# Kernel tuning notes

Hardware: AMD Instinct MI355X
Metric: run time of the kernel (lower is better)

The kernel has to match this reference:

```python
import jax, jax.numpy as jnp
import numpy as np

V0, V1, C = 64, 128, 128
V = V0 * V1  # product-graph node count = kron eigenvalue count


def setup_inputs() -> dict:
    key = jax.random.key(0)
    ks = jax.random.split(key, 8)
    x = jax.random.normal(ks[0], (V, C), dtype=jnp.float32)
    edge_index = jax.random.randint(ks[1], (2, 100), 0, V)  # unused on spectral path
    L = jnp.zeros((2, 2), dtype=jnp.float32)                # unused on spectral path
    mass = jax.random.uniform(ks[2], (V,), dtype=jnp.float32) + 0.5  # positive lumped mass
    evals0 = jax.random.uniform(ks[3], (V0,), dtype=jnp.float32) * 2.0  # factor-graph eigenvalues >= 0
    evals1 = jax.random.uniform(ks[4], (V1,), dtype=jnp.float32) * 2.0
    evecs = jax.random.normal(ks[5], (V, V), dtype=jnp.float32) / np.float32(np.sqrt(V))
    diffusion_time = jax.random.uniform(ks[6], (2, C), dtype=jnp.float32)  # nn.Parameter [P, C_inout]
    return {
        "x": x, "edge_index": edge_index, "L": L, "mass": mass,
        "evals0": evals0, "evals1": evals1, "evecs": evecs,
        "diffusion_time": diffusion_time,
    }


def reference(x, edge_index, L, mass, evals0, evals1, evecs, diffusion_time):
    # to_basis: project mass-weighted signal onto the spectral basis. [V,C]
    x_spec = evecs.T @ (x * mass[:, None])
    # Per-channel Kronecker diffusion coefficients:
    # kron(exp(-t0[c]*evals0), exp(-t1[c]*evals1)) for each channel c.
    e0 = jnp.exp(-evals0[:, None] * diffusion_time[0][None, :])  # [V0, C]
    e1 = jnp.exp(-evals1[:, None] * diffusion_time[1][None, :])  # [V1, C]
    diffusion_coefs = (e0[:, None, :] * e1[None, :, :]).reshape(V0 * V1, C)  # [V, C]
    # from_basis: back to node domain.
    x_diffuse = evecs @ (diffusion_coefs * x_spec)
    return x_diffuse
```

## Files before the change

### kernel.cpp

```cpp
#include <hip/hip_runtime.h>
#include <hip/hip_bf16.h>
#include <stdint.h>

#define V 8192
#define C 128
#define KS 8
#define KCH (V / KS)
#define BK 64
#define NI (KCH / BK)

typedef __attribute__((ext_vector_type(8))) short short8;
typedef __attribute__((ext_vector_type(4))) float floatx4;

static __device__ __forceinline__ unsigned short f2bf(float f) {
    unsigned u = __float_as_uint(f);
    u += 0x7FFF + ((u >> 16) & 1);
    return (unsigned short)(u >> 16);
}

__global__ __launch_bounds__(256) void prep_xmt(const float* __restrict__ x,
                                                const float* __restrict__ mass,
                                                unsigned short* __restrict__ XMT) {
    __shared__ float tile[64][65];
    const int k0 = blockIdx.x * 64;
    const int c0 = blockIdx.y * 64;
    const int t = threadIdx.x;
#pragma unroll
    for (int p = 0; p < 16; ++p) {
        int idx = p * 256 + t;
        int kk = idx >> 6, cc = idx & 63;
        tile[kk][cc] = x[(size_t)(k0 + kk) * C + (c0 + cc)] * mass[k0 + kk];
    }
    __syncthreads();
#pragma unroll
    for (int p = 0; p < 16; ++p) {
        int idx = p * 256 + t;
        int cc = idx >> 6, kk = idx & 63;
        XMT[(size_t)(c0 + cc) * V + (k0 + kk)] = f2bf(tile[kk][cc]);
    }
}

#define MFMA_BODY                                                                   \
    {                                                                               \
        _Pragma("unroll")                                                           \
        for (int kk = 0; kk < BK; kk += 32) {                                       \
            short8 af[4], bf[4];                                                    \
            _Pragma("unroll")                                                       \
            for (int mi = 0; mi < 4; ++mi) {                                        \
                int m = wm + mi * 16 + l15;                                         \
                int cpos = ((kk >> 3) + q) ^ (m & 7);                               \
                af[mi] = *(const short8*)&ldsA[m * BK + 8 * cpos];                  \
            }                                                                       \
            _Pragma("unroll")                                                       \
            for (int ni = 0; ni < 4; ++ni) {                                        \
                int n = wn + ni * 16 + l15;                                         \
                int cpos = ((kk >> 3) + q) ^ (n & 7);                               \
                bf[ni] = *(const short8*)&ldsB[n * BK + 8 * cpos];                  \
            }                                                                       \
            _Pragma("unroll")                                                       \
            for (int mi = 0; mi < 4; ++mi)                                          \
                _Pragma("unroll")                                                   \
                for (int ni = 0; ni < 4; ++ni)                                      \
                    acc[mi][ni] = __builtin_amdgcn_mfma_f32_16x16x32_bf16(          \
                        af[mi], bf[ni], acc[mi][ni], 0, 0, 0);                      \
        }                                                                           \
    }

__global__ __launch_bounds__(256, 2) void gemm1_fused(const unsigned short* __restrict__ XMT,
                                                      const float* __restrict__ E,
                                                      float* __restrict__ P1) {
    __shared__ __align__(16) unsigned short ldsA[128 * BK];
    __shared__ __align__(16) unsigned short ldsB[128 * BK];
    const int bx = blockIdx.x;
    const int ks = bx & (KS - 1);
    const int n0 = (bx >> 3) * 128;
    const int kb = ks * KCH;
    const int t = threadIdx.x;
    const int w = t >> 6, lane = t & 63, q = lane >> 4, l15 = lane & 15;
    const int wm = (w & 1) * 64, wn = (w >> 1) * 64;
    const int acp = t & 7;
    const int ar8 = t >> 3;
    const int jg = (t & 7) | ((t >> 6) << 3);
    const int vq = (t >> 3) & 7;

    floatx4 acc[4][4] = {};
    float4 e0[8], e1[8];

#pragma unroll
    for (int rr = 0; rr < 8; ++rr)
        e0[rr] = *(const float4*)&E[(size_t)(kb + vq * 8 + rr) * V + n0 + jg * 4];

    for (int it = 0; it < NI; it += 2) {
        const int k0 = kb + it * BK;
        const int k1 = k0 + BK;
        const int kp = (k1 + BK < kb + KCH) ? (k1 + BK) : (kb + KCH - BK);
        __syncthreads();
        uint4 br[4];
#pragma unroll
        for (int u = 0; u < 4; ++u)
            br[u] = *(const uint4*)&XMT[(size_t)(ar8 + 32 * u) * V + k0 + acp * 8];
#pragma unroll
        for (int rr = 0; rr < 8; ++rr)
            e1[rr] = *(const float4*)&E[(size_t)(k1 + vq * 8 + rr) * V + n0 + jg * 4];
#pragma unroll
        for (int u = 0; u < 4; ++u) {
            int r = ar8 + 32 * u;
            *(uint4*)&ldsA[r * BK + ((acp ^ (r & 7))) * 8] = br[u];
        }
        {
            const float* lf = (const float*)e0;
#pragma unroll
            for (int jj = 0; jj < 4; ++jj) {
                int j = jg * 4 + jj;
                short8 b;
#pragma unroll
                for (int rr = 0; rr < 8; ++rr) b[rr] = (short)f2bf(lf[rr * 4 + jj]);
                *(short8*)&ldsB[j * BK + (vq ^ (j & 7)) * 8] = b;
            }
        }
        __syncthreads();
        MFMA_BODY;
        __syncthreads();
#pragma unroll
        for (int u = 0; u < 4; ++u)
            br[u] = *(const uint4*)&XMT[(size_t)(ar8 + 32 * u) * V + k1 + acp * 8];
#pragma unroll
        for (int rr = 0; rr < 8; ++rr)
            e0[rr] = *(const float4*)&E[(size_t)(kp + vq * 8 + rr) * V + n0 + jg * 4];
#pragma unroll
        for (int u = 0; u < 4; ++u) {
            int r = ar8 + 32 * u;
            *(uint4*)&ldsA[r * BK + ((acp ^ (r & 7))) * 8] = br[u];
        }
        {
            const float* lf = (const float*)e1;
#pragma unroll
            for (int jj = 0; jj < 4; ++jj) {
                int j = jg * 4 + jj;
                short8 b;
#pragma unroll
                for (int rr = 0; rr < 8; ++rr) b[rr] = (short)f2bf(lf[rr * 4 + jj]);
                *(short8*)&ldsB[j * BK + (vq ^ (j & 7)) * 8] = b;
            }
        }
        __syncthreads();
        MFMA_BODY;
    }
    float* Pks = P1 + (size_t)ks * C * V;
#pragma unroll
    for (int mi = 0; mi < 4; ++mi) {
        int mrow = wm + mi * 16 + q * 4;
#pragma unroll
        for (int ni = 0; ni < 4; ++ni) {
            int n = n0 + wn + ni * 16 + l15;
#pragma unroll
            for (int r = 0; r < 4; ++r)
                Pks[(size_t)(mrow + r) * V + n] = acc[mi][ni][r];
        }
    }
}

__global__ __launch_bounds__(256, 2) void gemm2_fused(const float* __restrict__ E,
                                                      const unsigned short* __restrict__ YT,
                                                      float* __restrict__ P2) {
    __shared__ __align__(16) unsigned short ldsA[128 * BK];
    __shared__ __align__(16) unsigned short ldsB[128 * BK];
    const int bx = blockIdx.x;
    const int ks = bx & (KS - 1);
    const int m0 = (bx >> 3) * 128;
    const int kb = ks * KCH;
    const int t = threadIdx.x;
    const int w = t >> 6, lane = t & 63, q = lane >> 4, l15 = lane & 15;
    const int wm = (w & 1) * 64, wn = (w >> 1) * 64;
    const int ach = t & 15;
    const int ar  = t >> 4;
    const int bcp = t & 7;
    const int br8 = t >> 3;

    floatx4 acc[4][4] = {};
    float4 e0[8], e1[8];

#pragma unroll
    for (int u = 0; u < 8; ++u)
        e0[u] = *(const float4*)&E[(size_t)(m0 + ar + 16 * u) * V + kb + ach * 4];

    for (int it = 0; it < NI; it += 2) {
        const int k0 = kb + it * BK;
        const int k1 = k0 + BK;
        const int kp = (k1 + BK < kb + KCH) ? (k1 + BK) : (kb + KCH - BK);
        __syncthreads();
        uint4 br[4];
#pragma unroll
        for (int u = 0; u < 4; ++u)
            br[u] = *(const uint4*)&YT[(size_t)(br8 + 32 * u) * V + k0 + bcp * 8];
#pragma unroll
        for (int u = 0; u < 8; ++u)
            e1[u] = *(const float4*)&E[(size_t)(m0 + ar + 16 * u) * V + k1 + ach * 4];
#pragma unroll
        for (int u = 0; u < 4; ++u) {
            int r = br8 + 32 * u;
            *(uint4*)&ldsB[r * BK + ((bcp ^ (r & 7))) * 8] = br[u];
        }
        {
            const float* lf = (const float*)e0;
#pragma unroll
            for (int u = 0; u < 8; ++u) {
                int row = ar + 16 * u;
                ushort4 av;
                av.x = f2bf(lf[u * 4 + 0]); av.y = f2bf(lf[u * 4 + 1]);
                av.z = f2bf(lf[u * 4 + 2]); av.w = f2bf(lf[u * 4 + 3]);
                *(ushort4*)&ldsA[row * BK + ((ach >> 1) ^ (row & 7)) * 8 + (ach & 1) * 4] = av;
            }
        }
        __syncthreads();
        MFMA_BODY;
        __syncthreads();
#pragma unroll
        for (int u = 0; u < 4; ++u)
            br[u] = *(const uint4*)&YT[(size_t)(br8 + 32 * u) * V + k1 + bcp * 8];
#pragma unroll
        for (int u = 0; u < 8; ++u)
            e0[u] = *(const float4*)&E[(size_t)(m0 + ar + 16 * u) * V + kp + ach * 4];
#pragma unroll
        for (int u = 0; u < 4; ++u) {
            int r = br8 + 32 * u;
            *(uint4*)&ldsB[r * BK + ((bcp ^ (r & 7))) * 8] = br[u];
        }
        {
            const float* lf = (const float*)e1;
#pragma unroll
            for (int u = 0; u < 8; ++u) {
                int row = ar + 16 * u;
                ushort4 av;
                av.x = f2bf(lf[u * 4 + 0]); av.y = f2bf(lf[u * 4 + 1]);
                av.z = f2bf(lf[u * 4 + 2]); av.w = f2bf(lf[u * 4 + 3]);
                *(ushort4*)&ldsA[row * BK + ((ach >> 1) ^ (row & 7)) * 8 + (ach & 1) * 4] = av;
            }
        }
        __syncthreads();
        MFMA_BODY;
    }
    float* Pks = P2 + (size_t)ks * V * C;
#pragma unroll
    for (int mi = 0; mi < 4; ++mi) {
        int mrow = m0 + wm + mi * 16 + q * 4;
#pragma unroll
        for (int ni = 0; ni < 4; ++ni) {
            int n = wn + ni * 16 + l15;
#pragma unroll
            for (int r = 0; r < 4; ++r)
                Pks[(size_t)(mrow + r) * C + n] = acc[mi][ni][r];
        }
    }
}

__global__ __launch_bounds__(256) void red1(const float* __restrict__ P1,
                                            const float* __restrict__ ev0,
                                            const float* __restrict__ ev1,
                                            const float* __restrict__ dt,
                                            unsigned short* __restrict__ YT) {
    int id = blockIdx.x * 256 + threadIdx.x;
    int c = id >> 10;
    int j0 = (id & 1023) * 8;
    float s[8] = {};
#pragma unroll
    for (int ks = 0; ks < KS; ++ks) {
        const float* row = &P1[((size_t)ks * C + c) * V + j0];
        float4 a = *(const float4*)row;
        float4 b = *(const float4*)(row + 4);
        s[0] += a.x; s[1] += a.y; s[2] += a.z; s[3] += a.w;
        s[4] += b.x; s[5] += b.y; s[6] += b.z; s[7] += b.w;
    }
    float t0 = dt[c], t1 = dt[C + c];
    float a0 = ev0[j0 >> 7] * t0;
    short8 yv;
#pragma unroll
    for (int jj = 0; jj < 8; ++jj) {
        float coef = __expf(-(a0 + ev1[(j0 + jj) & 127] * t1));
        yv[jj] = (short)f2bf(s[jj] * coef);
    }
    *(short8*)&YT[(size_t)c * V + j0] = yv;
}

__global__ __launch_bounds__(256) void red2(const float* __restrict__ P2,
                                            float* __restrict__ out) {
    int id = blockIdx.x * 256 + threadIdx.x;
    size_t off = (size_t)id * 4;
    float4 s = {0.f, 0.f, 0.f, 0.f};
#pragma unroll
    for (int ks = 0; ks < KS; ++ks) {
        float4 v = *(const float4*)&P2[(size_t)ks * V * C + off];
        s.x += v.x; s.y += v.y; s.z += v.z; s.w += v.w;
    }
    *(float4*)&out[off] = s;
}

extern "C" void kernel_launch(void* const* d_in, const int* in_sizes, int n_in,
                              void* d_out, int out_size, void* d_ws, size_t ws_size,
                              hipStream_t stream) {
    const float* x    = (const float*)d_in[0];
    const float* mass = (const float*)d_in[3];
    const float* ev0  = (const float*)d_in[4];
    const float* ev1  = (const float*)d_in[5];
    const float* E    = (const float*)d_in[6];
    const float* dt   = (const float*)d_in[7];
    float* out = (float*)d_out;

    unsigned short* XMT = (unsigned short*)d_ws;
    unsigned short* YT  = XMT + (size_t)V * C;
    float* P = (float*)(YT + (size_t)V * C);

    prep_xmt<<<dim3(V / 64, C / 64), 256, 0, stream>>>(x, mass, XMT);
    gemm1_fused<<<(V / 128) * KS, 256, 0, stream>>>(XMT, E, P);
    red1<<<(C * V / 8) / 256, 256, 0, stream>>>(P, ev0, ev1, dt, YT);
    gemm2_fused<<<(V / 128) * KS, 256, 0, stream>>>(E, YT, P);
    red2<<<(V * C / 4) / 256, 256, 0, stream>>>(P, out);
}
```

Baseline: 444.3 us.

## Double-buffer LDS and use direct global-to-LDS loads in both GEMMs

Both split-K GEMM kernels now keep two LDS buffers and prefetch the next K tile while MFMAs run on the current one. The bf16 operand tile is loaded with global_load_lds straight into LDS, with the XOR swizzle folded into the source address. The fp32 E tile is still staged in registers and converted after compute. The loop is rewritten with one barrier per iteration, explicit waitcnt, sched_barrier and setprio around the MFMA body, which removes the extra syncs and register staging. In exchange, LDS use per block doubles to 64 KB, which may limit occupancy.

After: 447.8 us. Within noise of the previous version (+0.8%).

```diff
diff --git a/kernel.cpp b/kernel.cpp
--- a/kernel.cpp
+++ b/kernel.cpp
@@ -1,5 +1,4 @@
 #include <hip/hip_runtime.h>
-#include <hip/hip_bf16.h>
 #include <stdint.h>
 
 #define V 8192
@@ -17,6 +16,13 @@
     u += 0x7FFF + ((u >> 16) & 1);
     return (unsigned short)(u >> 16);
 }
+
+static __device__ __forceinline__ void gload16(const void* g, void* l) {
+    __builtin_amdgcn_global_load_lds(
+        (const __attribute__((address_space(1))) void*)g,
+        (__attribute__((address_space(3))) void*)l, 16, 0, 0);
+}
+#define SWAIT(s) asm volatile("s_waitcnt " s ::: "memory")
 
 __global__ __launch_bounds__(256) void prep_xmt(const float* __restrict__ x,
                                                 const float* __restrict__ mass,
@@ -40,37 +46,37 @@
     }
 }
 
-#define MFMA_BODY                                                                   \
+#define MFMA_BODY(pA, pB)                                                           \
     {                                                                               \
         _Pragma("unroll")                                                           \
         for (int kk = 0; kk < BK; kk += 32) {                                       \
-            short8 af[4], bf[4];                                                    \
+            short8 af[4], bfv[4];                                                   \
             _Pragma("unroll")                                                       \
             for (int mi = 0; mi < 4; ++mi) {                                        \
-                int m = wm + mi * 16 + l15;                                         \
-                int cpos = ((kk >> 3) + q) ^ (m & 7);                               \
-                af[mi] = *(const short8*)&ldsA[m * BK + 8 * cpos];                  \
+                const int m = wm + mi * 16 + l15;                                   \
+                const int cpos = ((kk >> 3) + q) ^ (m & 7);                         \
+                af[mi] = *(const short8*)&pA[m * BK + 8 * cpos];                    \
             }                                                                       \
             _Pragma("unroll")                                                       \
             for (int ni = 0; ni < 4; ++ni) {                                        \
-                int n = wn + ni * 16 + l15;                                         \
-                int cpos = ((kk >> 3) + q) ^ (n & 7);                               \
-                bf[ni] = *(const short8*)&ldsB[n * BK + 8 * cpos];                  \
+                const int n = wn + ni * 16 + l15;                                   \
+                const int cpos = ((kk >> 3) + q) ^ (n & 7);                         \
+                bfv[ni] = *(const short8*)&pB[n * BK + 8 * cpos];                   \
             }                                                                       \
             _Pragma("unroll")                                                       \
             for (int mi = 0; mi < 4; ++mi)                                          \
                 _Pragma("unroll")                                                   \
                 for (int ni = 0; ni < 4; ++ni)                                      \
                     acc[mi][ni] = __builtin_amdgcn_mfma_f32_16x16x32_bf16(          \
-                        af[mi], bf[ni], acc[mi][ni], 0, 0, 0);                      \
+                        af[mi], bfv[ni], acc[mi][ni], 0, 0, 0);                     \
         }                                                                           \
     }
 
 __global__ __launch_bounds__(256, 2) void gemm1_fused(const unsigned short* __restrict__ XMT,
                                                       const float* __restrict__ E,
                                                       float* __restrict__ P1) {
-    __shared__ __align__(16) unsigned short ldsA[128 * BK];
-    __shared__ __align__(16) unsigned short ldsB[128 * BK];
+    __shared__ __align__(16) unsigned short ldsA[2][128 * BK];
+    __shared__ __align__(16) unsigned short ldsB[2][128 * BK];
     const int bx = blockIdx.x;
     const int ks = bx & (KS - 1);
     const int n0 = (bx >> 3) * 128;
@@ -78,74 +84,76 @@
     const int t = threadIdx.x;
     const int w = t >> 6, lane = t & 63, q = lane >> 4, l15 = lane & 15;
     const int wm = (w & 1) * 64, wn = (w >> 1) * 64;
-    const int acp = t & 7;
-    const int ar8 = t >> 3;
-    const int jg = (t & 7) | ((t >> 6) << 3);
-    const int vq = (t >> 3) & 7;
+    const int lr = lane >> 3;
+    const int lch = (lane & 7) ^ lr;
+    const int jg = (lane & 7) | (w << 3);
+    const int vq = lane >> 3;
 
     floatx4 acc[4][4] = {};
-    float4 e0[8], e1[8];
-
-#pragma unroll
-    for (int rr = 0; rr < 8; ++rr)
-        e0[rr] = *(const float4*)&E[(size_t)(kb + vq * 8 + rr) * V + n0 + jg * 4];
-
-    for (int it = 0; it < NI; it += 2) {
-        const int k0 = kb + it * BK;
-        const int k1 = k0 + BK;
-        const int kp = (k1 + BK < kb + KCH) ? (k1 + BK) : (kb + KCH - BK);
-        __syncthreads();
-        uint4 br[4];
-#pragma unroll
-        for (int u = 0; u < 4; ++u)
-            br[u] = *(const uint4*)&XMT[(size_t)(ar8 + 32 * u) * V + k0 + acp * 8];
+    float4 ereg[8];
+
+    {
+        const int k0 = kb;
+#pragma unroll
+        for (int i = 0; i < 4; ++i)
+            gload16(&XMT[(size_t)(i * 32 + w * 8 + lr) * V + k0 + 8 * lch],
+                    &ldsA[0][i * 2048 + w * 512]);
 #pragma unroll
         for (int rr = 0; rr < 8; ++rr)
-            e1[rr] = *(const float4*)&E[(size_t)(k1 + vq * 8 + rr) * V + n0 + jg * 4];
-#pragma unroll
-        for (int u = 0; u < 4; ++u) {
-            int r = ar8 + 32 * u;
-            *(uint4*)&ldsA[r * BK + ((acp ^ (r & 7))) * 8] = br[u];
-        }
+            ereg[rr] = *(const float4*)&E[(size_t)(k0 + vq * 8 + rr) * V + n0 + jg * 4];
+        const float* lf = (const float*)ereg;
+#pragma unroll
+        for (int jj = 0; jj < 4; ++jj) {
+            const int j = jg * 4 + jj;
+            short8 b;
+#pragma unroll
+            for (int rr = 0; rr < 8; ++rr) b[rr] = (short)f2bf(lf[rr * 4 + jj]);
+            *(short8*)&ldsB[0][j * BK + (vq ^ (j & 7)) * 8] = b;
+        }
+        SWAIT("vmcnt(0) lgkmcnt(0)");
+        __builtin_amdgcn_s_barrier();
+        __builtin_amdgcn_sched_barrier(0);
+    }
+
+    int cur = 0;
+    for (int tt = 0; tt < NI; ++tt) {
+        const bool pf = (tt + 1 < NI);
+        if (pf) {
+            const int kn = kb + (tt + 1) * BK;
+#pragma unroll
+            for (int i = 0; i < 4; ++i)
+                gload16(&XMT[(size_t)(i * 32 + w * 8 + lr) * V + kn + 8 * lch],
+                        &ldsA[cur ^ 1][i * 2048 + w * 512]);
+#pragma unroll
+            for (int rr = 0; rr < 8; ++rr)
+                ereg[rr] = *(const float4*)&E[(size_t)(kn + vq * 8 + rr) * V + n0 + jg * 4];
+        }
+        __builtin_amdgcn_sched_barrier(0);
         {
-            const float* lf = (const float*)e0;
+            const unsigned short* pA = ldsA[cur];
+            const unsigned short* pB = ldsB[cur];
+            __builtin_amdgcn_s_setprio(1);
+            MFMA_BODY(pA, pB);
+            __builtin_amdgcn_s_setprio(0);
+        }
+        __builtin_amdgcn_sched_barrier(0);
+        if (pf) {
+            const float* lf = (const float*)ereg;
 #pragma unroll
             for (int jj = 0; jj < 4; ++jj) {
-                int j = jg * 4 + jj;
+                const int j = jg * 4 + jj;
                 short8 b;
 #pragma unroll
                 for (int rr = 0; rr < 8; ++rr) b[rr] = (short)f2bf(lf[rr * 4 + jj]);
-                *(short8*)&ldsB[j * BK + (vq ^ (j & 7)) * 8] = b;
+                *(short8*)&ldsB[cur ^ 1][j * BK + (vq ^ (j & 7)) * 8] = b;
             }
         }
-        __syncthreads();
-        MFMA_BODY;
-        __syncthreads();
-#pragma unroll
-        for (int u = 0; u < 4; ++u)
-            br[u] = *(const uint4*)&XMT[(size_t)(ar8 + 32 * u) * V + k1 + acp * 8];
-#pragma unroll
-        for (int rr = 0; rr < 8; ++rr)
-            e0[rr] = *(const float4*)&E[(size_t)(kp + vq * 8 + rr) * V + n0 + jg * 4];
-#pragma unroll
-        for (int u = 0; u < 4; ++u) {
-            int r = ar8 + 32 * u;
-            *(uint4*)&ldsA[r * BK + ((acp ^ (r & 7))) * 8] = br[u];
-        }
-        {
-            const float* lf = (const float*)e1;
-#pragma unroll
-            for (int jj = 0; jj < 4; ++jj) {
-                int j = jg * 4 + jj;
-                short8 b;
-#pragma unroll
-                for (int rr = 0; rr < 8; ++rr) b[rr] = (short)f2bf(lf[rr * 4 + jj]);
-                *(short8*)&ldsB[j * BK + (vq ^ (j & 7)) * 8] = b;
-            }
-        }
-        __syncthreads();
-        MFMA_BODY;
-    }
+        SWAIT("vmcnt(0) lgkmcnt(0)");
+        __builtin_amdgcn_s_barrier();
+        __builtin_amdgcn_sched_barrier(0);
+        cur ^= 1;
+    }
+
     float* Pks = P1 + (size_t)ks * C * V;
 #pragma unroll
     for (int mi = 0; mi < 4; ++mi) {
@@ -163,8 +171,8 @@
 __global__ __launch_bounds__(256, 2) void gemm2_fused(const float* __restrict__ E,
                                                       const unsigned short* __restrict__ YT,
                                                       float* __restrict__ P2) {
-    __shared__ __align__(16) unsigned short ldsA[128 * BK];
-    __shared__ __align__(16) unsigned short ldsB[128 * BK];
+    __shared__ __align__(16) unsigned short ldsA[2][128 * BK];
+    __shared__ __align__(16) unsigned short ldsB[2][128 * BK];
     const int bx = blockIdx.x;
     const int ks = bx & (KS - 1);
     const int m0 = (bx >> 3) * 128;
@@ -172,74 +180,76 @@
     const int t = threadIdx.x;
     const int w = t >> 6, lane = t & 63, q = lane >> 4, l15 = lane & 15;
     const int wm = (w & 1) * 64, wn = (w >> 1) * 64;
+    const int lr = lane >> 3;
+    const int lch = (lane & 7) ^ lr;
     const int ach = t & 15;
     const int ar  = t >> 4;
-    const int bcp = t & 7;
-    const int br8 = t >> 3;
 
     floatx4 acc[4][4] = {};
-    float4 e0[8], e1[8];
-
-#pragma unroll
-    for (int u = 0; u < 8; ++u)
-        e0[u] = *(const float4*)&E[(size_t)(m0 + ar + 16 * u) * V + kb + ach * 4];
-
-    for (int it = 0; it < NI; it += 2) {
-        const int k0 = kb + it * BK;
-        const int k1 = k0 + BK;
-        const int kp = (k1 + BK < kb + KCH) ? (k1 + BK) : (kb + KCH - BK);
-        __syncthreads();
-        uint4 br[4];
-#pragma unroll
-        for (int u = 0; u < 4; ++u)
-            br[u] = *(const uint4*)&YT[(size_t)(br8 + 32 * u) * V + k0 + bcp * 8];
+    float4 ereg[8];
+
+    {
+        const int k0 = kb;
+#pragma unroll
+        for (int i = 0; i < 4; ++i)
+            gload16(&YT[(size_t)(i * 32 + w * 8 + lr) * V + k0 + 8 * lch],
+                    &ldsB[0][i * 2048 + w * 512]);
 #pragma unroll
         for (int u = 0; u < 8; ++u)
-            e1[u] = *(const float4*)&E[(size_t)(m0 + ar + 16 * u) * V + k1 + ach * 4];
-#pragma unroll
-        for (int u = 0; u < 4; ++u) {
-            int r = br8 + 32 * u;
-            *(uint4*)&ldsB[r * BK + ((bcp ^ (r & 7))) * 8] = br[u];
-        }
+            ereg[u] = *(const float4*)&E[(size_t)(m0 + ar + 16 * u) * V + k0 + ach * 4];
+        const float* lf = (const float*)ereg;
+#pragma unroll
+        for (int u = 0; u < 8; ++u) {
+            const int row = ar + 16 * u;
+            ushort4 av;
+            av.x = f2bf(lf[u * 4 + 0]); av.y = f2bf(lf[u * 4 + 1]);
+            av.z = f2bf(lf[u * 4 + 2]); av.w = f2bf(lf[u * 4 + 3]);
+            *(ushort4*)&ldsA[0][row * BK + ((ach >> 1) ^ (row & 7)) * 8 + (ach & 1) * 4] = av;
+        }
+        SWAIT("vmcnt(0) lgkmcnt(0)");
+        __builtin_amdgcn_s_barrier();
+        __builtin_amdgcn_sched_barrier(0);
+    }
+
+    int cur = 0;
+    for (int tt = 0; tt < NI; ++tt) {
+        const bool pf = (tt + 1 < NI);
+        if (pf) {
+            const int kn = kb + (tt + 1) * BK;
+#pragma unroll
+            for (int i = 0; i < 4; ++i)
+                gload16(&YT[(size_t)(i * 32 + w * 8 + lr) * V + kn + 8 * lch],
+                        &ldsB[cur ^ 1][i * 2048 + w * 512]);
+#pragma unroll
+            for (int u = 0; u < 8; ++u)
+                ereg[u] = *(const float4*)&E[(size_t)(m0 + ar + 16 * u) * V + kn + ach * 4];
+        }
+        __builtin_amdgcn_sched_barrier(0);
         {
-            const float* lf = (const float*)e0;
+            const unsigned short* pA = ldsA[cur];
+            const unsigned short* pB = ldsB[cur];
+            __builtin_amdgcn_s_setprio(1);
+            MFMA_BODY(pA, pB);
+            __builtin_amdgcn_s_setprio(0);
+        }
+        __builtin_amdgcn_sched_barrier(0);
+        if (pf) {
+            const float* lf = (const float*)ereg;
 #pragma unroll
             for (int u = 0; u < 8; ++u) {
-                int row = ar + 16 * u;
+                const int row = ar + 16 * u;
                 ushort4 av;
                 av.x = f2bf(lf[u * 4 + 0]); av.y = f2bf(lf[u * 4 + 1]);
                 av.z = f2bf(lf[u * 4 + 2]); av.w = f2bf(lf[u * 4 + 3]);
-                *(ushort4*)&ldsA[row * BK + ((ach >> 1) ^ (row & 7)) * 8 + (ach & 1) * 4] = av;
+                *(ushort4*)&ldsA[cur ^ 1][row * BK + ((ach >> 1) ^ (row & 7)) * 8 + (ach & 1) * 4] = av;
             }
         }
-        __syncthreads();
-        MFMA_BODY;
-        __syncthreads();
-#pragma unroll
-        for (int u = 0; u < 4; ++u)
-            br[u] = *(const uint4*)&YT[(size_t)(br8 + 32 * u) * V + k1 + bcp * 8];
-#pragma unroll
-        for (int u = 0; u < 8; ++u)
-            e0[u] = *(const float4*)&E[(size_t)(m0 + ar + 16 * u) * V + kp + ach * 4];
-#pragma unroll
-        for (int u = 0; u < 4; ++u) {
-            int r = br8 + 32 * u;
-            *(uint4*)&ldsB[r * BK + ((bcp ^ (r & 7))) * 8] = br[u];
-        }
-        {
-            const float* lf = (const float*)e1;
-#pragma unroll
-            for (int u = 0; u < 8; ++u) {
-                int row = ar + 16 * u;
-                ushort4 av;
-                av.x = f2bf(lf[u * 4 + 0]); av.y = f2bf(lf[u * 4 + 1]);
-                av.z = f2bf(lf[u * 4 + 2]); av.w = f2bf(lf[u * 4 + 3]);
-                *(ushort4*)&ldsA[row * BK + ((ach >> 1) ^ (row & 7)) * 8 + (ach & 1) * 4] = av;
-            }
-        }
-        __syncthreads();
-        MFMA_BODY;
-    }
+        SWAIT("vmcnt(0) lgkmcnt(0)");
+        __builtin_amdgcn_s_barrier();
+        __builtin_amdgcn_sched_barrier(0);
+        cur ^= 1;
+    }
+
     float* Pks = P2 + (size_t)ks * V * C;
 #pragma unroll
     for (int mi = 0; mi < 4; ++mi) {
```
